# Performance work log

Hardware: AMD Instinct MI355X
Metric: run time of the kernel (lower is better)

Reference implementation:

```python
import jax, jax.numpy as jnp
import numpy as np

B = 1024       # batch of graphs
NUM = 512      # predicates / nodes per graph
D = 64         # embedding_dim
H = 64         # hidden_dim
E = 4096       # edges per graph (shared structure across batch)
MAIN_NUM = 10  # softmax segment [0, MAIN_NUM); sigmoid on the rest


def setup_inputs() -> dict:
    key = jax.random.key(0)
    ks = jax.random.split(key, 8)
    x = jax.random.uniform(ks[0], (B, NUM), dtype=jnp.float32)
    embedding = jax.random.normal(ks[1], (NUM, D), dtype=jnp.float32) * 0.1
    W1 = jax.random.normal(ks[2], (D, H), dtype=jnp.float32) * (1.0 / np.sqrt(D))
    b1 = jnp.zeros((H,), jnp.float32)
    W2 = jax.random.normal(ks[3], (H, H), dtype=jnp.float32) * (1.0 / np.sqrt(H))
    b2 = jnp.zeros((H,), jnp.float32)
    W3 = jax.random.normal(ks[4], (H, 1), dtype=jnp.float32) * (1.0 / np.sqrt(H))
    b3 = jnp.zeros((1,), jnp.float32)
    edge_row = jax.random.randint(ks[5], (E,), 0, NUM, dtype=jnp.int32)
    edge_col = jax.random.randint(ks[6], (E,), 0, NUM, dtype=jnp.int32)
    return {"x": x, "embedding": embedding, "W1": W1, "b1": b1,
            "W2": W2, "b2": b2, "W3": W3, "b3": b3,
            "edge_row": edge_row, "edge_col": edge_col}


def _gcn_layer(h, W, b, row, col, norm):
    # h: [B, NUM, in]; GCNConv = linear -> D^{-1/2} A D^{-1/2} aggregate -> +bias
    hW = jnp.einsum('bni,io->bno', h, W)                 # [B, NUM, out]
    msg = hW[:, row, :] * norm[None, :, None]            # [B, E, out]
    agg = jnp.zeros_like(hW).at[:, col, :].add(msg)      # scatter to targets
    return agg + b


def reference(x, embedding, W1, b1, W2, b2, W3, b3, edge_row, edge_col):
    num = x.shape[1]
    # symmetric GCN normalization (add_self_loops=False, unit edge weights)
    deg = jnp.zeros((num,), x.dtype).at[edge_col].add(1.0)
    dinv = jnp.where(deg > 0, jax.lax.rsqrt(jnp.maximum(deg, 1.0)), 0.0)
    norm = dinv[edge_row] * dinv[edge_col]               # [E]

    h = x[..., None] * embedding                         # [B, NUM, D]
    h = jax.nn.relu(_gcn_layer(h, W1, b1, edge_row, edge_col, norm))
    h = jax.nn.relu(_gcn_layer(h, W2, b2, edge_row, edge_col, norm))
    logits = _gcn_layer(h, W3, b3, edge_row, edge_col, norm)[..., 0]  # [B, NUM]

    # convert_to_confidence: softmax over multiclass segment, sigmoid elsewhere
    phi_sm = jax.nn.softmax(logits[:, :MAIN_NUM], axis=1)
    phi_sg = jax.nn.sigmoid(logits[:, MAIN_NUM:])
    return jnp.concatenate([phi_sm, phi_sg], axis=1)
```

## Files before the change

### kernel.cpp

```cpp
#include <hip/hip_runtime.h>
#include <stdint.h>

#define NB    1024
#define NUM   512
#define HD    64
#define NE    4096
#define NEP   4608
#define MAIN  10
#define HBS   72

typedef _Float16 hlf;
typedef __attribute__((ext_vector_type(2))) _Float16 hlf2;
typedef __attribute__((ext_vector_type(8))) _Float16 hlf8;
typedef __attribute__((ext_vector_type(4))) float f32x4;

__device__ __forceinline__ unsigned short f2h(float f) {
    hlf v = (hlf)f;
    return __builtin_bit_cast(unsigned short, v);
}

__global__ __launch_bounds__(512) void prep_all(
    const int* __restrict__ erow, const int* __restrict__ ecol,
    const float* __restrict__ emb, const float* __restrict__ W1,
    const float* __restrict__ W2,
    int* __restrict__ rsptr, int* __restrict__ colmap, int* __restrict__ epk,
    short* __restrict__ E1, short* __restrict__ W2T)
{
    const int t = threadIdx.x;
    if (blockIdx.x != 0) {
        int g = (blockIdx.x - 1) * 512 + t;
        if (g < NUM * HD) {
            int node = g >> 6, dim = g & 63;
            float acc = 0.0f;
            #pragma unroll
            for (int k = 0; k < HD; ++k) acc += emb[node * HD + k] * W1[k * HD + dim];
            E1[g] = (short)f2h(acc);
        } else if (g < NUM * HD + HD * HD) {
            int j = g - NUM * HD;
            int dout = j >> 6, din = j & 63;
            W2T[j] = (short)f2h(W2[din * HD + dout]);
        }
        return;
    }

    __shared__ int   sdeg[NUM];
    __shared__ int   aux[NUM];
    __shared__ float sdv[NUM];
    __shared__ int   rnk[NUM];
    __shared__ int   rdg[NUM];
    __shared__ int   wsum[8];

    const int lane = t & 63, wv = t >> 6;

    sdeg[t] = 0; aux[t] = 0;
    __syncthreads();
    for (int e = t; e < NE; e += 512) atomicAdd(&sdeg[ecol[e]], 1);
    __syncthreads();
    const int deg  = sdeg[t];
    const int pdeg = (deg + 1) & ~1;
    const int dbin = deg < NUM ? deg : NUM - 1;
    sdv[t] = deg > 0 ? rsqrtf((float)deg) : 0.0f;
    atomicAdd(&aux[dbin], 1);
    __syncthreads();
    {
        int v = aux[t];
        #pragma unroll
        for (int ofs = 1; ofs < 64; ofs <<= 1) {
            int sh = __shfl_up(v, ofs, 64);
            if (lane >= ofs) v += sh;
        }
        if (lane == 63) wsum[wv] = v;
        __syncthreads();
        if (t == 0) {
            int s = 0;
            #pragma unroll
            for (int w = 0; w < 8; ++w) { int tmp = wsum[w]; wsum[w] = s; s += tmp; }
        }
        __syncthreads();
        int inc = v + wsum[wv];
        aux[t]  = inc;
        __syncthreads();
        sdeg[t] = (t == 0) ? 0 : aux[t - 1];
        __syncthreads();
    }
    {
        int r = atomicAdd(&sdeg[dbin], 1);
        rnk[t] = r;
        rdg[r] = pdeg;
        colmap[r] = t;
    }
    __syncthreads();
    {
        int dv = rdg[t], v = dv;
        #pragma unroll
        for (int ofs = 1; ofs < 64; ofs <<= 1) {
            int sh = __shfl_up(v, ofs, 64);
            if (lane >= ofs) v += sh;
        }
        if (lane == 63) wsum[wv] = v;
        __syncthreads();
        if (t == 0) {
            int s = 0;
            #pragma unroll
            for (int w = 0; w < 8; ++w) { int tmp = wsum[w]; wsum[w] = s; s += tmp; }
        }
        __syncthreads();
        int inc  = v + wsum[wv];
        int excl = inc - dv;
        rsptr[t] = excl;
        if (t == NUM - 1) rsptr[NUM] = inc;
        aux[t] = excl;
        __syncthreads();
    }
    sdeg[t] = aux[rnk[t]];
    __syncthreads();
    for (int i = t; i < NEP; i += 512) epk[i] = 0;
    __syncthreads();
    for (int e = t; e < NE; e += 512) {
        int c = ecol[e], rr = erow[e];
        int p = atomicAdd(&sdeg[c], 1);
        unsigned ns = (unsigned)f2h(sdv[rr] * sdv[c]);
        epk[p] = (rr << 23) | (int)ns;
    }
}

__global__ __launch_bounds__(1024, 4) void gcn_body(
    const float* __restrict__ x, const hlf* __restrict__ E1,
    const hlf* __restrict__ W2T,
    const float* __restrict__ b1, const float* __restrict__ b2,
    const float* __restrict__ W3, const float* __restrict__ b3,
    const int* __restrict__ rsptrg, const int* __restrict__ colmap,
    const int* __restrict__ epkg,
    float* __restrict__ out)
{
    __shared__ hlf HA[NUM * HD];
    __shared__ hlf HB[NUM * HBS];
    __shared__ int eps[NEP + 8];
    __shared__ int sptr[513];
    __shared__ float sred[2];

    float* tv   = (float*)HB;
    float* slog = ((float*)HB) + NUM;

    const int t     = threadIdx.x;
    const int b     = blockIdx.x;
    const int lane  = t & 63;
    const int wave  = t >> 6;
    const int q     = lane >> 4;
    const int l15   = lane & 15;
    const int grp   = lane >> 3;
    const int dbase = (lane & 7) * 8;

    {
        const int4* g4 = (const int4*)epkg;
        *(int4*)&eps[t * 4] = g4[t];
        if (t < 128) *(int4*)&eps[4096 + t * 4] = g4[1024 + t];
        if (t < 8)   eps[NEP + t] = 0;
    }
    if (t < 513) sptr[t] = rsptrg[t];

    #pragma unroll
    for (int p = 0; p < 4; ++p) {
        int i = t + p * 1024;
        int r = i >> 3, d8 = (i & 7) * 8;
        float xr = x[b * NUM + r];
        hlf  xh = (hlf)xr;
        hlf8 e  = *(const hlf8*)&E1[r * HD + d8];
        hlf8 o;
        #pragma unroll
        for (int j = 0; j < 8; ++j) o[j] = e[j] * xh;
        *(hlf8*)&HA[r * HD + d8] = o;
    }

    float b1v[8], b2v[8], w3v[8];
    {
        f32x4 u0 = *(const f32x4*)&b1[dbase], u1 = *(const f32x4*)&b1[dbase + 4];
        f32x4 v0 = *(const f32x4*)&b2[dbase], v1 = *(const f32x4*)&b2[dbase + 4];
        f32x4 w0 = *(const f32x4*)&W3[dbase], w1 = *(const f32x4*)&W3[dbase + 4];
        #pragma unroll
        for (int j = 0; j < 4; ++j) {
            b1v[j] = u0[j]; b1v[j + 4] = u1[j];
            b2v[j] = v0[j]; b2v[j + 4] = v1[j];
            w3v[j] = w0[j]; w3v[j + 4] = w1[j];
        }
    }
    const char* HAb = (const char*)HA + dbase * 2;
    __syncthreads();

#define LDROW(d, pe) d = *(const uint4*)(HAb + ((unsigned)(pe) >> 16));
#define MACROW(hv, pe) {                                                      \
        const hlf nh = __builtin_bit_cast(hlf2, (unsigned)(pe))[0];           \
        const hlf2 p0 = __builtin_bit_cast(hlf2, (hv).x);                     \
        const hlf2 p1 = __builtin_bit_cast(hlf2, (hv).y);                     \
        const hlf2 p2 = __builtin_bit_cast(hlf2, (hv).z);                     \
        const hlf2 p3 = __builtin_bit_cast(hlf2, (hv).w);                     \
        a[0] = fmaf((float)p0[0], (float)nh, a[0]);                           \
        a[1] = fmaf((float)p0[1], (float)nh, a[1]);                           \
        a[2] = fmaf((float)p1[0], (float)nh, a[2]);                           \
        a[3] = fmaf((float)p1[1], (float)nh, a[3]);                           \
        a[4] = fmaf((float)p2[0], (float)nh, a[4]);                           \
        a[5] = fmaf((float)p2[1], (float)nh, a[5]);                           \
        a[6] = fmaf((float)p3[0], (float)nh, a[6]);                           \
        a[7] = fmaf((float)p3[1], (float)nh, a[7]); }

#define SPMM_PIPE(E0, E1v)                                                    \
    int e = E0;                                                               \
    int2 qa0 = *(const int2*)&eps[e], qb0 = *(const int2*)&eps[e + 2];        \
    uint4 u0, u1, u2, u3;                                                     \
    LDROW(u0, qa0.x) LDROW(u1, qa0.y) LDROW(u2, qb0.x) LDROW(u3, qb0.y)       \
    for (; e + 4 < E1v; e += 4) {                                             \
        int2 qa1 = *(const int2*)&eps[e + 4];                                 \
        int2 qb1 = *(const int2*)&eps[e + 6];                                 \
        uint4 w0, w1, w2, w3;                                                 \
        LDROW(w0, qa1.x) LDROW(w1, qa1.y) LDROW(w2, qb1.x) LDROW(w3, qb1.y)   \
        MACROW(u0, qa0.x) MACROW(u1, qa0.y)                                   \
        MACROW(u2, qb0.x) MACROW(u3, qb0.y)                                   \
        qa0 = qa1; qb0 = qb1; u0 = w0; u1 = w1; u2 = w2; u3 = w3;             \
    }                                                                         \
    if (e < E1v)     { MACROW(u0, qa0.x) MACROW(u1, qa0.y) }                  \
    if (e + 2 < E1v) { MACROW(u2, qb0.x) MACROW(u3, qb0.y) }

    #pragma unroll 1
    for (int set = 0; set < 4; ++set) {
        int wv8 = ((set & 1) ? (15 - wave) : wave) * 8;
        int r  = set * 128 + wv8 + grp;
        int e0 = sptr[r], e1 = sptr[r + 1];
        int c  = colmap[r];
        float a[8];
        #pragma unroll
        for (int j = 0; j < 8; ++j) a[j] = 0.0f;
        { SPMM_PIPE(e0, e1) }
        uint4 ov;
        ov.x = __builtin_bit_cast(unsigned, __builtin_amdgcn_cvt_pkrtz(
                   fmaxf(a[0] + b1v[0], 0.0f), fmaxf(a[1] + b1v[1], 0.0f)));
        ov.y = __builtin_bit_cast(unsigned, __builtin_amdgcn_cvt_pkrtz(
                   fmaxf(a[2] + b1v[2], 0.0f), fmaxf(a[3] + b1v[3], 0.0f)));
        ov.z = __builtin_bit_cast(unsigned, __builtin_amdgcn_cvt_pkrtz(
                   fmaxf(a[4] + b1v[4], 0.0f), fmaxf(a[5] + b1v[5], 0.0f)));
        ov.w = __builtin_bit_cast(unsigned, __builtin_amdgcn_cvt_pkrtz(
                   fmaxf(a[6] + b1v[6], 0.0f), fmaxf(a[7] + b1v[7], 0.0f)));
        *(uint4*)&HB[c * HBS + dbase] = ov;
    }
    __syncthreads();

    {
        hlf8 bfr[2][4];
        #pragma unroll
        for (int ks = 0; ks < 2; ++ks)
            #pragma unroll
            for (int nt = 0; nt < 4; ++nt)
                bfr[ks][nt] = *(const hlf8*)&W2T[(nt * 16 + l15) * HD + ks * 32 + q * 8];
        f32x4 acc[2][4];
        #pragma unroll
        for (int mt = 0; mt < 2; ++mt)
            #pragma unroll
            for (int nt = 0; nt < 4; ++nt) acc[mt][nt] = (f32x4){0.f, 0.f, 0.f, 0.f};
        const int mbase = wave * 32;
        #pragma unroll
        for (int mt = 0; mt < 2; ++mt)
            #pragma unroll
            for (int ks = 0; ks < 2; ++ks) {
                hlf8 af = *(const hlf8*)&HB[(mbase + mt * 16 + l15) * HBS
                                            + ks * 32 + q * 8];
                #pragma unroll
                for (int nt = 0; nt < 4; ++nt)
                    acc[mt][nt] = __builtin_amdgcn_mfma_f32_16x16x32_f16(
                        af, bfr[ks][nt], acc[mt][nt], 0, 0, 0);
            }
        #pragma unroll
        for (int mt = 0; mt < 2; ++mt)
            #pragma unroll
            for (int nt = 0; nt < 4; ++nt)
                #pragma unroll
                for (int i = 0; i < 4; ++i)
                    HA[(mbase + mt * 16 + q * 4 + i) * HD + nt * 16 + l15] =
                        (hlf)acc[mt][nt][i];
    }
    __syncthreads();

    #pragma unroll 1
    for (int set = 0; set < 4; ++set) {
        int wv8 = ((set & 1) ? (15 - wave) : wave) * 8;
        int r  = set * 128 + wv8 + grp;
        int e0 = sptr[r], e1 = sptr[r + 1];
        int c  = colmap[r];
        float a[8];
        #pragma unroll
        for (int j = 0; j < 8; ++j) a[j] = 0.0f;
        { SPMM_PIPE(e0, e1) }
        float v = 0.0f;
        #pragma unroll
        for (int j = 0; j < 8; ++j)
            v += fmaxf(a[j] + b2v[j], 0.0f) * w3v[j];
        v += __shfl_xor(v, 1, 64);
        v += __shfl_xor(v, 2, 64);
        v += __shfl_xor(v, 4, 64);
        if ((lane & 7) == 0) tv[c] = v;
    }
    __syncthreads();

    {
        int rk = t >> 1, hh = t & 1;
        int e0 = sptr[rk], e1 = sptr[rk + 1];
        int mid = (e0 + e1) >> 1;
        int ea = hh ? mid : e0;
        int eb = hh ? e1 : mid;
        float acc = 0.0f;
        for (int e = ea; e < eb; ++e) {
            unsigned pe = (unsigned)eps[e];
            float nf = (float)__builtin_bit_cast(hlf2, pe)[0];
            acc = fmaf(nf, *(const float*)((const char*)tv + (pe >> 21)), acc);
        }
        acc += __shfl_xor(acc, 1, 64);
        if (!hh) slog[colmap[rk]] = acc + b3[0];
    }
    __syncthreads();

    if (t < 64) {
        float v = (t < MAIN) ? slog[t] : -1e30f;
        float m = v;
        m = fmaxf(m, __shfl_xor(m, 1, 64));
        m = fmaxf(m, __shfl_xor(m, 2, 64));
        m = fmaxf(m, __shfl_xor(m, 4, 64));
        m = fmaxf(m, __shfl_xor(m, 8, 64));
        float ev = (t < MAIN) ? __expf(v - m) : 0.0f;
        ev += __shfl_xor(ev, 1, 64);
        ev += __shfl_xor(ev, 2, 64);
        ev += __shfl_xor(ev, 4, 64);
        ev += __shfl_xor(ev, 8, 64);
        if (t == 0) { sred[0] = m; sred[1] = ev; }
    }
    __syncthreads();

    if (t < NUM) {
        float l = slog[t];
        float o = (t < MAIN) ? __expf(l - sred[0]) / sred[1]
                             : 1.0f / (1.0f + __expf(-l));
        out[b * NUM + t] = o;
    }
#undef LDROW
#undef MACROW
#undef SPMM_PIPE
}

extern "C" void kernel_launch(void* const* d_in, const int* in_sizes, int n_in,
                              void* d_out, int out_size, void* d_ws, size_t ws_size,
                              hipStream_t stream) {
    const float* x    = (const float*)d_in[0];
    const float* emb  = (const float*)d_in[1];
    const float* W1   = (const float*)d_in[2];
    const float* b1   = (const float*)d_in[3];
    const float* W2   = (const float*)d_in[4];
    const float* b2   = (const float*)d_in[5];
    const float* W3   = (const float*)d_in[6];
    const float* b3   = (const float*)d_in[7];
    const int*   erow = (const int*)d_in[8];
    const int*   ecol = (const int*)d_in[9];

    char* ws = (char*)d_ws;
    int*   rsptr  = (int*)ws;
    int*   colmap = (int*)(ws + 2176);
    int*   epk    = (int*)(ws + 4224);
    short* E1     = (short*)(ws + 22656);
    short* W2T    = (short*)(ws + 88192);

    prep_all<<<73, 512, 0, stream>>>(erow, ecol, emb, W1, W2,
                                     rsptr, colmap, epk, E1, W2T);
    gcn_body<<<NB, 1024, 0, stream>>>(x, (const hlf*)E1, (const hlf*)W2T,
                                      b1, b2, W3, b3,
                                      rsptr, colmap, epk, (float*)d_out);
}
```

Baseline: 158.5 us.

## Reorder GCN stages to aggregate before transform and shrink shared memory

Layer 1 now gathers rows of the precomputed embedding·W1 table straight from global memory, scaling each edge by x times the edge norm, so the per-graph scaled embedding copy in LDS is no longer built. Layer 2 aggregates first and then runs the MFMA transform, fusing bias, ReLU and the W3 dot product into the MFMA epilogue, which removes the third SpMM over 64 features. Edge pointers, column map and degree are packed into one descriptor word, edges are read from global memory instead of being staged in LDS, and the row buffer uses an XOR swizzle instead of padding. Together these cut LDS use enough to raise the launch bound to 8 waves per SIMD, at the cost of more global and L2 gather traffic and the loss of the software-pipelined gather loop.

```diff
diff --git a/kernel.cpp b/kernel.cpp
--- a/kernel.cpp
+++ b/kernel.cpp
@@ -7,7 +7,6 @@
 #define NE    4096
 #define NEP   4608
 #define MAIN  10
-#define HBS   72
 
 typedef _Float16 hlf;
 typedef __attribute__((ext_vector_type(2))) _Float16 hlf2;
@@ -23,7 +22,7 @@
     const int* __restrict__ erow, const int* __restrict__ ecol,
     const float* __restrict__ emb, const float* __restrict__ W1,
     const float* __restrict__ W2,
-    int* __restrict__ rsptr, int* __restrict__ colmap, int* __restrict__ epk,
+    unsigned* __restrict__ desc, int* __restrict__ epk,
     short* __restrict__ E1, short* __restrict__ W2T)
 {
     const int t = threadIdx.x;
@@ -48,6 +47,7 @@
     __shared__ float sdv[NUM];
     __shared__ int   rnk[NUM];
     __shared__ int   rdg[NUM];
+    __shared__ int   scol[NUM];
     __shared__ int   wsum[8];
 
     const int lane = t & 63, wv = t >> 6;
@@ -87,7 +87,7 @@
         int r = atomicAdd(&sdeg[dbin], 1);
         rnk[t] = r;
         rdg[r] = pdeg;
-        colmap[r] = t;
+        scol[r] = t;
     }
     __syncthreads();
     {
@@ -107,8 +107,7 @@
         __syncthreads();
         int inc  = v + wsum[wv];
         int excl = inc - dv;
-        rsptr[t] = excl;
-        if (t == NUM - 1) rsptr[NUM] = inc;
+        desc[t] = (unsigned)excl | ((unsigned)scol[t] << 13) | ((unsigned)dv << 22);
         aux[t] = excl;
         __syncthreads();
     }
@@ -124,23 +123,20 @@
     }
 }
 
-__global__ __launch_bounds__(1024, 4) void gcn_body(
+__global__ __launch_bounds__(1024, 8) void gcn_body(
     const float* __restrict__ x, const hlf* __restrict__ E1,
     const hlf* __restrict__ W2T,
     const float* __restrict__ b1, const float* __restrict__ b2,
     const float* __restrict__ W3, const float* __restrict__ b3,
-    const int* __restrict__ rsptrg, const int* __restrict__ colmap,
-    const int* __restrict__ epkg,
+    const unsigned* __restrict__ descg, const int* __restrict__ epkg,
     float* __restrict__ out)
 {
-    __shared__ hlf HA[NUM * HD];
-    __shared__ hlf HB[NUM * HBS];
-    __shared__ int eps[NEP + 8];
-    __shared__ int sptr[513];
-    __shared__ float sred[2];
-
-    float* tv   = (float*)HB;
-    float* slog = ((float*)HB) + NUM;
+    __shared__ hlf   H[NUM * HD];
+    __shared__ float aux[NUM];
+    __shared__ hlf   xe[NEP];
+
+    float* slog = (float*)H;
+    float* sred = ((float*)H) + NUM;
 
     const int t     = threadIdx.x;
     const int b     = blockIdx.x;
@@ -149,170 +145,162 @@
     const int q     = lane >> 4;
     const int l15   = lane & 15;
     const int grp   = lane >> 3;
-    const int dbase = (lane & 7) * 8;
-
-    {
-        const int4* g4 = (const int4*)epkg;
-        *(int4*)&eps[t * 4] = g4[t];
-        if (t < 128) *(int4*)&eps[4096 + t * 4] = g4[1024 + t];
-        if (t < 8)   eps[NEP + t] = 0;
-    }
-    if (t < 513) sptr[t] = rsptrg[t];
-
-    #pragma unroll
-    for (int p = 0; p < 4; ++p) {
-        int i = t + p * 1024;
-        int r = i >> 3, d8 = (i & 7) * 8;
-        float xr = x[b * NUM + r];
-        hlf  xh = (hlf)xr;
-        hlf8 e  = *(const hlf8*)&E1[r * HD + d8];
-        hlf8 o;
-        #pragma unroll
-        for (int j = 0; j < 8; ++j) o[j] = e[j] * xh;
-        *(hlf8*)&HA[r * HD + d8] = o;
-    }
-
-    float b1v[8], b2v[8], w3v[8];
+    const int l7    = lane & 7;
+    const int dbase = l7 * 8;
+
+    if (t < NUM) aux[t] = x[b * NUM + t];
+    __syncthreads();
+    for (int i = t; i < NEP; i += 1024) {
+        unsigned pe = (unsigned)epkg[i];
+        float nf = (float)__builtin_bit_cast(hlf2, pe)[0];
+        xe[i] = (hlf)(nf * aux[pe >> 23]);
+    }
+
+    float b1v[8];
     {
         f32x4 u0 = *(const f32x4*)&b1[dbase], u1 = *(const f32x4*)&b1[dbase + 4];
-        f32x4 v0 = *(const f32x4*)&b2[dbase], v1 = *(const f32x4*)&b2[dbase + 4];
-        f32x4 w0 = *(const f32x4*)&W3[dbase], w1 = *(const f32x4*)&W3[dbase + 4];
-        #pragma unroll
-        for (int j = 0; j < 4; ++j) {
-            b1v[j] = u0[j]; b1v[j + 4] = u1[j];
-            b2v[j] = v0[j]; b2v[j + 4] = v1[j];
-            w3v[j] = w0[j]; w3v[j + 4] = w1[j];
-        }
-    }
-    const char* HAb = (const char*)HA + dbase * 2;
-    __syncthreads();
-
-#define LDROW(d, pe) d = *(const uint4*)(HAb + ((unsigned)(pe) >> 16));
-#define MACROW(hv, pe) {                                                      \
-        const hlf nh = __builtin_bit_cast(hlf2, (unsigned)(pe))[0];           \
+        #pragma unroll
+        for (int j = 0; j < 4; ++j) { b1v[j] = u0[j]; b1v[j + 4] = u1[j]; }
+    }
+    __syncthreads();
+
+#define MAC8(hv, sc) {                                                        \
         const hlf2 p0 = __builtin_bit_cast(hlf2, (hv).x);                     \
         const hlf2 p1 = __builtin_bit_cast(hlf2, (hv).y);                     \
         const hlf2 p2 = __builtin_bit_cast(hlf2, (hv).z);                     \
         const hlf2 p3 = __builtin_bit_cast(hlf2, (hv).w);                     \
-        a[0] = fmaf((float)p0[0], (float)nh, a[0]);                           \
-        a[1] = fmaf((float)p0[1], (float)nh, a[1]);                           \
-        a[2] = fmaf((float)p1[0], (float)nh, a[2]);                           \
-        a[3] = fmaf((float)p1[1], (float)nh, a[3]);                           \
-        a[4] = fmaf((float)p2[0], (float)nh, a[4]);                           \
-        a[5] = fmaf((float)p2[1], (float)nh, a[5]);                           \
-        a[6] = fmaf((float)p3[0], (float)nh, a[6]);                           \
-        a[7] = fmaf((float)p3[1], (float)nh, a[7]); }
-
-#define SPMM_PIPE(E0, E1v)                                                    \
-    int e = E0;                                                               \
-    int2 qa0 = *(const int2*)&eps[e], qb0 = *(const int2*)&eps[e + 2];        \
-    uint4 u0, u1, u2, u3;                                                     \
-    LDROW(u0, qa0.x) LDROW(u1, qa0.y) LDROW(u2, qb0.x) LDROW(u3, qb0.y)       \
-    for (; e + 4 < E1v; e += 4) {                                             \
-        int2 qa1 = *(const int2*)&eps[e + 4];                                 \
-        int2 qb1 = *(const int2*)&eps[e + 6];                                 \
-        uint4 w0, w1, w2, w3;                                                 \
-        LDROW(w0, qa1.x) LDROW(w1, qa1.y) LDROW(w2, qb1.x) LDROW(w3, qb1.y)   \
-        MACROW(u0, qa0.x) MACROW(u1, qa0.y)                                   \
-        MACROW(u2, qb0.x) MACROW(u3, qb0.y)                                   \
-        qa0 = qa1; qb0 = qb1; u0 = w0; u1 = w1; u2 = w2; u3 = w3;             \
-    }                                                                         \
-    if (e < E1v)     { MACROW(u0, qa0.x) MACROW(u1, qa0.y) }                  \
-    if (e + 2 < E1v) { MACROW(u2, qb0.x) MACROW(u3, qb0.y) }
-
-    #pragma unroll 1
-    for (int set = 0; set < 4; ++set) {
-        int wv8 = ((set & 1) ? (15 - wave) : wave) * 8;
-        int r  = set * 128 + wv8 + grp;
-        int e0 = sptr[r], e1 = sptr[r + 1];
-        int c  = colmap[r];
-        float a[8];
-        #pragma unroll
-        for (int j = 0; j < 8; ++j) a[j] = 0.0f;
-        { SPMM_PIPE(e0, e1) }
-        uint4 ov;
-        ov.x = __builtin_bit_cast(unsigned, __builtin_amdgcn_cvt_pkrtz(
-                   fmaxf(a[0] + b1v[0], 0.0f), fmaxf(a[1] + b1v[1], 0.0f)));
-        ov.y = __builtin_bit_cast(unsigned, __builtin_amdgcn_cvt_pkrtz(
-                   fmaxf(a[2] + b1v[2], 0.0f), fmaxf(a[3] + b1v[3], 0.0f)));
-        ov.z = __builtin_bit_cast(unsigned, __builtin_amdgcn_cvt_pkrtz(
-                   fmaxf(a[4] + b1v[4], 0.0f), fmaxf(a[5] + b1v[5], 0.0f)));
-        ov.w = __builtin_bit_cast(unsigned, __builtin_amdgcn_cvt_pkrtz(
-                   fmaxf(a[6] + b1v[6], 0.0f), fmaxf(a[7] + b1v[7], 0.0f)));
-        *(uint4*)&HB[c * HBS + dbase] = ov;
-    }
-    __syncthreads();
-
-    {
-        hlf8 bfr[2][4];
-        #pragma unroll
-        for (int ks = 0; ks < 2; ++ks)
-            #pragma unroll
-            for (int nt = 0; nt < 4; ++nt)
-                bfr[ks][nt] = *(const hlf8*)&W2T[(nt * 16 + l15) * HD + ks * 32 + q * 8];
-        f32x4 acc[2][4];
+        a[0] = fmaf((float)p0[0], (float)(sc), a[0]);                         \
+        a[1] = fmaf((float)p0[1], (float)(sc), a[1]);                         \
+        a[2] = fmaf((float)p1[0], (float)(sc), a[2]);                         \
+        a[3] = fmaf((float)p1[1], (float)(sc), a[3]);                         \
+        a[4] = fmaf((float)p2[0], (float)(sc), a[4]);                         \
+        a[5] = fmaf((float)p2[1], (float)(sc), a[5]);                         \
+        a[6] = fmaf((float)p3[0], (float)(sc), a[6]);                         \
+        a[7] = fmaf((float)p3[1], (float)(sc), a[7]); }
+
+    {
+        const char* E1b = (const char*)E1 + dbase * 2;
+        #pragma unroll 1
+        for (int set = 0; set < 4; ++set) {
+            int r = set * 128 + wave * 8 + grp;
+            unsigned d = descg[r];
+            int e0 = d & 8191, c = (d >> 13) & 511, e1 = e0 + (d >> 22);
+            float a[8];
+            #pragma unroll
+            for (int j = 0; j < 8; ++j) a[j] = 0.0f;
+            for (int e = e0; e < e1; e += 2) {
+                int2 qp = *(const int2*)&epkg[e];
+                hlf2 xs = *(const hlf2*)&xe[e];
+                uint4 g0 = *(const uint4*)(E1b + ((unsigned)qp.x >> 16));
+                uint4 g1 = *(const uint4*)(E1b + ((unsigned)qp.y >> 16));
+                MAC8(g0, xs[0]); MAC8(g1, xs[1]);
+            }
+            uint4 ov;
+            ov.x = __builtin_bit_cast(unsigned, __builtin_amdgcn_cvt_pkrtz(
+                       fmaxf(a[0] + b1v[0], 0.0f), fmaxf(a[1] + b1v[1], 0.0f)));
+            ov.y = __builtin_bit_cast(unsigned, __builtin_amdgcn_cvt_pkrtz(
+                       fmaxf(a[2] + b1v[2], 0.0f), fmaxf(a[3] + b1v[3], 0.0f)));
+            ov.z = __builtin_bit_cast(unsigned, __builtin_amdgcn_cvt_pkrtz(
+                       fmaxf(a[4] + b1v[4], 0.0f), fmaxf(a[5] + b1v[5], 0.0f)));
+            ov.w = __builtin_bit_cast(unsigned, __builtin_amdgcn_cvt_pkrtz(
+                       fmaxf(a[6] + b1v[6], 0.0f), fmaxf(a[7] + b1v[7], 0.0f)));
+            *(uint4*)&H[c * HD + dbase] = ov;
+        }
+    }
+    __syncthreads();
+
+    {
+        const char* Hb = (const char*)H + dbase * 2;
+        uint4 agg[4]; int cset[4];
+        #pragma unroll 1
+        for (int set = 0; set < 4; ++set) {
+            int r = set * 128 + wave * 8 + grp;
+            unsigned d = descg[r];
+            int e0 = d & 8191, c = (d >> 13) & 511, e1 = e0 + (d >> 22);
+            float a[8];
+            #pragma unroll
+            for (int j = 0; j < 8; ++j) a[j] = 0.0f;
+            for (int e = e0; e < e1; e += 2) {
+                int2 qp = *(const int2*)&epkg[e];
+                uint4 g0 = *(const uint4*)(Hb + ((unsigned)qp.x >> 16));
+                uint4 g1 = *(const uint4*)(Hb + ((unsigned)qp.y >> 16));
+                MAC8(g0, __builtin_bit_cast(hlf2, (unsigned)qp.x)[0]);
+                MAC8(g1, __builtin_bit_cast(hlf2, (unsigned)qp.y)[0]);
+            }
+            uint4 ov;
+            ov.x = __builtin_bit_cast(unsigned, __builtin_amdgcn_cvt_pkrtz(a[0], a[1]));
+            ov.y = __builtin_bit_cast(unsigned, __builtin_amdgcn_cvt_pkrtz(a[2], a[3]));
+            ov.z = __builtin_bit_cast(unsigned, __builtin_amdgcn_cvt_pkrtz(a[4], a[5]));
+            ov.w = __builtin_bit_cast(unsigned, __builtin_amdgcn_cvt_pkrtz(a[6], a[7]));
+            agg[set] = ov; cset[set] = c;
+        }
+        __syncthreads();
+        #pragma unroll
+        for (int set = 0; set < 4; ++set) {
+            int c = cset[set];
+            *(uint4*)((char*)H + c * 128 + ((dbase * 2) ^ ((c & 7) << 4))) = agg[set];
+        }
+    }
+    __syncthreads();
+
+    {
+        const int mbase = wave * 32;
+        const int sw0 = (q * 16) ^ ((l15 & 7) << 4);
+        const int sw1 = (64 + q * 16) ^ ((l15 & 7) << 4);
+        const char* rb0 = (const char*)H + (mbase + l15) * 128;
+        const char* rb1 = rb0 + 16 * 128;
+        hlf8 a00 = *(const hlf8*)(rb0 + sw0), a01 = *(const hlf8*)(rb0 + sw1);
+        hlf8 a10 = *(const hlf8*)(rb1 + sw0), a11 = *(const hlf8*)(rb1 + sw1);
+        float tp[2][4];
+        #pragma unroll
+        for (int i = 0; i < 4; ++i) { tp[0][i] = 0.0f; tp[1][i] = 0.0f; }
+        #pragma unroll
+        for (int nt = 0; nt < 4; ++nt) {
+            int col = nt * 16 + l15;
+            hlf8 bf0 = *(const hlf8*)&W2T[col * HD + q * 8];
+            hlf8 bf1 = *(const hlf8*)&W2T[col * HD + 32 + q * 8];
+            f32x4 acc0 = (f32x4){0.f, 0.f, 0.f, 0.f};
+            f32x4 acc1 = (f32x4){0.f, 0.f, 0.f, 0.f};
+            acc0 = __builtin_amdgcn_mfma_f32_16x16x32_f16(a00, bf0, acc0, 0, 0, 0);
+            acc0 = __builtin_amdgcn_mfma_f32_16x16x32_f16(a01, bf1, acc0, 0, 0, 0);
+            acc1 = __builtin_amdgcn_mfma_f32_16x16x32_f16(a10, bf0, acc1, 0, 0, 0);
+            acc1 = __builtin_amdgcn_mfma_f32_16x16x32_f16(a11, bf1, acc1, 0, 0, 0);
+            float bc = b2[col], wc = W3[col];
+            #pragma unroll
+            for (int i = 0; i < 4; ++i) {
+                tp[0][i] += fmaxf(acc0[i] + bc, 0.0f) * wc;
+                tp[1][i] += fmaxf(acc1[i] + bc, 0.0f) * wc;
+            }
+        }
         #pragma unroll
         for (int mt = 0; mt < 2; ++mt)
             #pragma unroll
-            for (int nt = 0; nt < 4; ++nt) acc[mt][nt] = (f32x4){0.f, 0.f, 0.f, 0.f};
-        const int mbase = wave * 32;
-        #pragma unroll
-        for (int mt = 0; mt < 2; ++mt)
-            #pragma unroll
-            for (int ks = 0; ks < 2; ++ks) {
-                hlf8 af = *(const hlf8*)&HB[(mbase + mt * 16 + l15) * HBS
-                                            + ks * 32 + q * 8];
-                #pragma unroll
-                for (int nt = 0; nt < 4; ++nt)
-                    acc[mt][nt] = __builtin_amdgcn_mfma_f32_16x16x32_f16(
-                        af, bfr[ks][nt], acc[mt][nt], 0, 0, 0);
+            for (int i = 0; i < 4; ++i) {
+                float v = tp[mt][i];
+                v += __shfl_xor(v, 1, 64);
+                v += __shfl_xor(v, 2, 64);
+                v += __shfl_xor(v, 4, 64);
+                v += __shfl_xor(v, 8, 64);
+                if (l15 == 0) aux[mbase + mt * 16 + q * 4 + i] = v;
             }
-        #pragma unroll
-        for (int mt = 0; mt < 2; ++mt)
-            #pragma unroll
-            for (int nt = 0; nt < 4; ++nt)
-                #pragma unroll
-                for (int i = 0; i < 4; ++i)
-                    HA[(mbase + mt * 16 + q * 4 + i) * HD + nt * 16 + l15] =
-                        (hlf)acc[mt][nt][i];
-    }
-    __syncthreads();
-
-    #pragma unroll 1
-    for (int set = 0; set < 4; ++set) {
-        int wv8 = ((set & 1) ? (15 - wave) : wave) * 8;
-        int r  = set * 128 + wv8 + grp;
-        int e0 = sptr[r], e1 = sptr[r + 1];
-        int c  = colmap[r];
-        float a[8];
-        #pragma unroll
-        for (int j = 0; j < 8; ++j) a[j] = 0.0f;
-        { SPMM_PIPE(e0, e1) }
-        float v = 0.0f;
-        #pragma unroll
-        for (int j = 0; j < 8; ++j)
-            v += fmaxf(a[j] + b2v[j], 0.0f) * w3v[j];
-        v += __shfl_xor(v, 1, 64);
-        v += __shfl_xor(v, 2, 64);
-        v += __shfl_xor(v, 4, 64);
-        if ((lane & 7) == 0) tv[c] = v;
     }
     __syncthreads();
 
     {
         int rk = t >> 1, hh = t & 1;
-        int e0 = sptr[rk], e1 = sptr[rk + 1];
-        int mid = (e0 + e1) >> 1;
+        unsigned d = descg[rk];
+        int e0 = d & 8191, c = (d >> 13) & 511, deg = d >> 22;
+        int mid = e0 + (deg >> 1);
         int ea = hh ? mid : e0;
-        int eb = hh ? e1 : mid;
+        int eb = hh ? e0 + deg : mid;
         float acc = 0.0f;
         for (int e = ea; e < eb; ++e) {
-            unsigned pe = (unsigned)eps[e];
+            unsigned pe = (unsigned)epkg[e];
             float nf = (float)__builtin_bit_cast(hlf2, pe)[0];
-            acc = fmaf(nf, *(const float*)((const char*)tv + (pe >> 21)), acc);
+            acc = fmaf(nf, aux[pe >> 23], acc);
         }
         acc += __shfl_xor(acc, 1, 64);
-        if (!hh) slog[colmap[rk]] = acc + b3[0];
+        if (!hh) slog[c] = acc + b3[0];
     }
     __syncthreads();
 
@@ -338,9 +326,7 @@
                              : 1.0f / (1.0f + __expf(-l));
         out[b * NUM + t] = o;
     }
-#undef LDROW
-#undef MACROW
-#undef SPMM_PIPE
+#undef MAC8
 }
 
 extern "C" void kernel_launch(void* const* d_in, const int* in_sizes, int n_in,
@@ -358,15 +344,14 @@
     const int*   ecol = (const int*)d_in[9];
 
     char* ws = (char*)d_ws;
-    int*   rsptr  = (int*)ws;
-    int*   colmap = (int*)(ws + 2176);
+    unsigned* desc = (unsigned*)ws;
     int*   epk    = (int*)(ws + 4224);
     short* E1     = (short*)(ws + 22656);
     short* W2T    = (short*)(ws + 88192);
 
     prep_all<<<73, 512, 0, stream>>>(erow, ecol, emb, W1, W2,
-                                     rsptr, colmap, epk, E1, W2T);
+                                     desc, epk, E1, W2T);
     gcn_body<<<NB, 1024, 0, stream>>>(x, (const hlf*)E1, (const hlf*)W2T,
                                       b1, b2, W3, b3,
-                                      rsptr, colmap, epk, (float*)d_out);
+                                      desc, epk, (float*)d_out);
 }
```

Result: slower. 170.5 us (+7.5%).

## Replace sparse gather aggregation with dense MFMA adjacency matmul

Applied to the files above, without the earlier changes.

Builds a dense normalized adjacency matrix (512x512) in the prep kernel via atomics, converts it to fp16 in an MFMA fragment layout, and computes the first two GCN aggregations as dense matrix multiplies on the matrix cores instead of per-edge LDS gathers. Node features are now stored transposed with XOR swizzling in LDS, and the layer-2 linear plus W3 projection are fused into one MFMA pass. This trades the irregular sparse gathers for about 64x more arithmetic (dense 512x512 versus 4096 edges). It also adds a memset and an extra cast kernel, and the dense fragments of S are streamed from global memory by every block.

```diff
diff --git a/kernel.cpp b/kernel.cpp
--- a/kernel.cpp
+++ b/kernel.cpp
@@ -7,7 +7,6 @@
 #define NE    4096
 #define NEP   4608
 #define MAIN  10
-#define HBS   72
 
 typedef _Float16 hlf;
 typedef __attribute__((ext_vector_type(2))) _Float16 hlf2;
@@ -24,17 +23,18 @@
     const float* __restrict__ emb, const float* __restrict__ W1,
     const float* __restrict__ W2,
     int* __restrict__ rsptr, int* __restrict__ colmap, int* __restrict__ epk,
-    short* __restrict__ E1, short* __restrict__ W2T)
+    short* __restrict__ E1T, short* __restrict__ W2T,
+    float* __restrict__ S32)
 {
     const int t = threadIdx.x;
     if (blockIdx.x != 0) {
         int g = (blockIdx.x - 1) * 512 + t;
         if (g < NUM * HD) {
-            int node = g >> 6, dim = g & 63;
+            int dim = g >> 9, node = g & 511;
             float acc = 0.0f;
             #pragma unroll
             for (int k = 0; k < HD; ++k) acc += emb[node * HD + k] * W1[k * HD + dim];
-            E1[g] = (short)f2h(acc);
+            E1T[g] = (short)f2h(acc);
         } else if (g < NUM * HD + HD * HD) {
             int j = g - NUM * HD;
             int dout = j >> 6, din = j & 63;
@@ -119,200 +119,217 @@
     for (int e = t; e < NE; e += 512) {
         int c = ecol[e], rr = erow[e];
         int p = atomicAdd(&sdeg[c], 1);
-        unsigned ns = (unsigned)f2h(sdv[rr] * sdv[c]);
-        epk[p] = (rr << 23) | (int)ns;
-    }
+        float nf = sdv[rr] * sdv[c];
+        unsigned ns = (unsigned)f2h(nf);
+        epk[p] = (rr << 16) | (int)ns;
+        atomicAdd(&S32[c * NUM + rr], nf);
+    }
+}
+
+__global__ __launch_bounds__(1024) void cast_S(
+    const float* __restrict__ S32, hlf* __restrict__ Sfr)
+{
+    int idx = blockIdx.x * 1024 + threadIdx.x;
+    int f = idx >> 6, l = idx & 63;
+    int mt = f >> 4, kt = f & 15;
+    int c  = mt * 16 + (l & 15);
+    int r0 = kt * 32 + (l >> 4) * 8;
+    const float* src = S32 + c * NUM + r0;
+    hlf8 o;
+    #pragma unroll
+    for (int j = 0; j < 8; ++j) o[j] = (hlf)src[j];
+    *(hlf8*)(Sfr + idx * 8) = o;
 }
 
 __global__ __launch_bounds__(1024, 4) void gcn_body(
-    const float* __restrict__ x, const hlf* __restrict__ E1,
-    const hlf* __restrict__ W2T,
+    const float* __restrict__ x, const hlf* __restrict__ E1T,
+    const hlf* __restrict__ W2T, const hlf* __restrict__ Sfr,
     const float* __restrict__ b1, const float* __restrict__ b2,
     const float* __restrict__ W3, const float* __restrict__ b3,
-    const int* __restrict__ rsptrg, const int* __restrict__ colmap,
+    const int* __restrict__ rsptrg, const int* __restrict__ cmapg,
     const int* __restrict__ epkg,
     float* __restrict__ out)
 {
-    __shared__ hlf HA[NUM * HD];
-    __shared__ hlf HB[NUM * HBS];
-    __shared__ int eps[NEP + 8];
-    __shared__ int sptr[513];
+    __shared__ hlf   HT[HD * NUM];
+    __shared__ hlf   AG[HD * NUM];
+    __shared__ float xs[NUM];
+    __shared__ float tv[NUM];
+    __shared__ float slog[NUM];
     __shared__ float sred[2];
 
-    float* tv   = (float*)HB;
-    float* slog = ((float*)HB) + NUM;
-
-    const int t     = threadIdx.x;
-    const int b     = blockIdx.x;
-    const int lane  = t & 63;
-    const int wave  = t >> 6;
-    const int q     = lane >> 4;
-    const int l15   = lane & 15;
-    const int grp   = lane >> 3;
-    const int dbase = (lane & 7) * 8;
-
-    {
-        const int4* g4 = (const int4*)epkg;
-        *(int4*)&eps[t * 4] = g4[t];
-        if (t < 128) *(int4*)&eps[4096 + t * 4] = g4[1024 + t];
-        if (t < 8)   eps[NEP + t] = 0;
-    }
-    if (t < 513) sptr[t] = rsptrg[t];
+    const int t    = threadIdx.x;
+    const int b    = blockIdx.x;
+    const int lane = t & 63;
+    const int wave = t >> 6;
+    const int q    = lane >> 4;
+    const int l15  = lane & 15;
+
+    if (t < NUM) xs[t] = x[b * NUM + t];
+    __syncthreads();
 
     #pragma unroll
     for (int p = 0; p < 4; ++p) {
         int i = t + p * 1024;
-        int r = i >> 3, d8 = (i & 7) * 8;
-        float xr = x[b * NUM + r];
-        hlf  xh = (hlf)xr;
-        hlf8 e  = *(const hlf8*)&E1[r * HD + d8];
+        int d = i >> 6, r0 = (i & 63) * 8;
+        hlf8 ev = *(const hlf8*)&E1T[d * NUM + r0];
         hlf8 o;
         #pragma unroll
-        for (int j = 0; j < 8; ++j) o[j] = e[j] * xh;
-        *(hlf8*)&HA[r * HD + d8] = o;
-    }
-
-    float b1v[8], b2v[8], w3v[8];
-    {
-        f32x4 u0 = *(const f32x4*)&b1[dbase], u1 = *(const f32x4*)&b1[dbase + 4];
-        f32x4 v0 = *(const f32x4*)&b2[dbase], v1 = *(const f32x4*)&b2[dbase + 4];
-        f32x4 w0 = *(const f32x4*)&W3[dbase], w1 = *(const f32x4*)&W3[dbase + 4];
-        #pragma unroll
-        for (int j = 0; j < 4; ++j) {
-            b1v[j] = u0[j]; b1v[j + 4] = u1[j];
-            b2v[j] = v0[j]; b2v[j + 4] = v1[j];
-            w3v[j] = w0[j]; w3v[j + 4] = w1[j];
-        }
-    }
-    const char* HAb = (const char*)HA + dbase * 2;
-    __syncthreads();
-
-#define LDROW(d, pe) d = *(const uint4*)(HAb + ((unsigned)(pe) >> 16));
-#define MACROW(hv, pe) {                                                      \
-        const hlf nh = __builtin_bit_cast(hlf2, (unsigned)(pe))[0];           \
-        const hlf2 p0 = __builtin_bit_cast(hlf2, (hv).x);                     \
-        const hlf2 p1 = __builtin_bit_cast(hlf2, (hv).y);                     \
-        const hlf2 p2 = __builtin_bit_cast(hlf2, (hv).z);                     \
-        const hlf2 p3 = __builtin_bit_cast(hlf2, (hv).w);                     \
-        a[0] = fmaf((float)p0[0], (float)nh, a[0]);                           \
-        a[1] = fmaf((float)p0[1], (float)nh, a[1]);                           \
-        a[2] = fmaf((float)p1[0], (float)nh, a[2]);                           \
-        a[3] = fmaf((float)p1[1], (float)nh, a[3]);                           \
-        a[4] = fmaf((float)p2[0], (float)nh, a[4]);                           \
-        a[5] = fmaf((float)p2[1], (float)nh, a[5]);                           \
-        a[6] = fmaf((float)p3[0], (float)nh, a[6]);                           \
-        a[7] = fmaf((float)p3[1], (float)nh, a[7]); }
-
-#define SPMM_PIPE(E0, E1v)                                                    \
-    int e = E0;                                                               \
-    int2 qa0 = *(const int2*)&eps[e], qb0 = *(const int2*)&eps[e + 2];        \
-    uint4 u0, u1, u2, u3;                                                     \
-    LDROW(u0, qa0.x) LDROW(u1, qa0.y) LDROW(u2, qb0.x) LDROW(u3, qb0.y)       \
-    for (; e + 4 < E1v; e += 4) {                                             \
-        int2 qa1 = *(const int2*)&eps[e + 4];                                 \
-        int2 qb1 = *(const int2*)&eps[e + 6];                                 \
-        uint4 w0, w1, w2, w3;                                                 \
-        LDROW(w0, qa1.x) LDROW(w1, qa1.y) LDROW(w2, qb1.x) LDROW(w3, qb1.y)   \
-        MACROW(u0, qa0.x) MACROW(u1, qa0.y)                                   \
-        MACROW(u2, qb0.x) MACROW(u3, qb0.y)                                   \
-        qa0 = qa1; qb0 = qb1; u0 = w0; u1 = w1; u2 = w2; u3 = w3;             \
-    }                                                                         \
-    if (e < E1v)     { MACROW(u0, qa0.x) MACROW(u1, qa0.y) }                  \
-    if (e + 2 < E1v) { MACROW(u2, qb0.x) MACROW(u3, qb0.y) }
-
-    #pragma unroll 1
-    for (int set = 0; set < 4; ++set) {
-        int wv8 = ((set & 1) ? (15 - wave) : wave) * 8;
-        int r  = set * 128 + wv8 + grp;
-        int e0 = sptr[r], e1 = sptr[r + 1];
-        int c  = colmap[r];
-        float a[8];
-        #pragma unroll
-        for (int j = 0; j < 8; ++j) a[j] = 0.0f;
-        { SPMM_PIPE(e0, e1) }
-        uint4 ov;
-        ov.x = __builtin_bit_cast(unsigned, __builtin_amdgcn_cvt_pkrtz(
-                   fmaxf(a[0] + b1v[0], 0.0f), fmaxf(a[1] + b1v[1], 0.0f)));
-        ov.y = __builtin_bit_cast(unsigned, __builtin_amdgcn_cvt_pkrtz(
-                   fmaxf(a[2] + b1v[2], 0.0f), fmaxf(a[3] + b1v[3], 0.0f)));
-        ov.z = __builtin_bit_cast(unsigned, __builtin_amdgcn_cvt_pkrtz(
-                   fmaxf(a[4] + b1v[4], 0.0f), fmaxf(a[5] + b1v[5], 0.0f)));
-        ov.w = __builtin_bit_cast(unsigned, __builtin_amdgcn_cvt_pkrtz(
-                   fmaxf(a[6] + b1v[6], 0.0f), fmaxf(a[7] + b1v[7], 0.0f)));
-        *(uint4*)&HB[c * HBS + dbase] = ov;
-    }
-    __syncthreads();
-
-    {
-        hlf8 bfr[2][4];
-        #pragma unroll
-        for (int ks = 0; ks < 2; ++ks)
+        for (int j = 0; j < 8; ++j) o[j] = ev[j] * (hlf)xs[r0 + j];
+        *(hlf8*)((char*)HT + d * 1024 + ((r0 * 2) ^ ((d & 7) << 4))) = o;
+    }
+
+    float b1l[4], b2l[4], w3l[4];
+    #pragma unroll
+    for (int nt = 0; nt < 4; ++nt) {
+        b1l[nt] = b1[nt * 16 + l15];
+        b2l[nt] = b2[nt * 16 + l15];
+        w3l[nt] = W3[nt * 16 + l15];
+    }
+    __syncthreads();
+
+    {
+        f32x4 acc[2][4];
+        #pragma unroll
+        for (int mm = 0; mm < 2; ++mm)
+            #pragma unroll
+            for (int nt = 0; nt < 4; ++nt) acc[mm][nt] = (f32x4){0.f, 0.f, 0.f, 0.f};
+        #pragma unroll
+        for (int kt = 0; kt < 16; ++kt) {
+            hlf8 bf[4];
+            #pragma unroll
+            for (int nt = 0; nt < 4; ++nt) {
+                int row = nt * 16 + l15;
+                bf[nt] = *(const hlf8*)((const char*)HT + row * 1024 +
+                             ((kt * 64 + q * 16) ^ ((row & 7) << 4)));
+            }
+            #pragma unroll
+            for (int mm = 0; mm < 2; ++mm) {
+                hlf8 af = *(const hlf8*)((const char*)Sfr +
+                              (((wave * 2 + mm) * 16 + kt) << 10) + lane * 16);
+                #pragma unroll
+                for (int nt = 0; nt < 4; ++nt)
+                    acc[mm][nt] = __builtin_amdgcn_mfma_f32_16x16x32_f16(
+                        af, bf[nt], acc[mm][nt], 0, 0, 0);
+            }
+        }
+        #pragma unroll
+        for (int mm = 0; mm < 2; ++mm) {
+            int mt = wave * 2 + mm;
+            #pragma unroll
+            for (int nt = 0; nt < 4; ++nt) {
+                int n = nt * 16 + l15;
+                uint2 pk;
+                pk.x = __builtin_bit_cast(unsigned, __builtin_amdgcn_cvt_pkrtz(
+                           fmaxf(acc[mm][nt][0] + b1l[nt], 0.0f),
+                           fmaxf(acc[mm][nt][1] + b1l[nt], 0.0f)));
+                pk.y = __builtin_bit_cast(unsigned, __builtin_amdgcn_cvt_pkrtz(
+                           fmaxf(acc[mm][nt][2] + b1l[nt], 0.0f),
+                           fmaxf(acc[mm][nt][3] + b1l[nt], 0.0f)));
+                *(uint2*)((char*)AG + n * 1024 +
+                          ((mt * 32 + q * 8) ^ ((n & 7) << 4))) = pk;
+            }
+        }
+    }
+    __syncthreads();
+
+    {
+        f32x4 acc[2][4];
+        #pragma unroll
+        for (int mm = 0; mm < 2; ++mm)
+            #pragma unroll
+            for (int nt = 0; nt < 4; ++nt) acc[mm][nt] = (f32x4){0.f, 0.f, 0.f, 0.f};
+        #pragma unroll
+        for (int kt = 0; kt < 16; ++kt) {
+            hlf8 bf[4];
+            #pragma unroll
+            for (int nt = 0; nt < 4; ++nt) {
+                int row = nt * 16 + l15;
+                bf[nt] = *(const hlf8*)((const char*)AG + row * 1024 +
+                             ((kt * 64 + q * 16) ^ ((row & 7) << 4)));
+            }
+            #pragma unroll
+            for (int mm = 0; mm < 2; ++mm) {
+                hlf8 af = *(const hlf8*)((const char*)Sfr +
+                              (((wave * 2 + mm) * 16 + kt) << 10) + lane * 16);
+                #pragma unroll
+                for (int nt = 0; nt < 4; ++nt)
+                    acc[mm][nt] = __builtin_amdgcn_mfma_f32_16x16x32_f16(
+                        af, bf[nt], acc[mm][nt], 0, 0, 0);
+            }
+        }
+        __syncthreads();
+        #pragma unroll
+        for (int mm = 0; mm < 2; ++mm) {
+            #pragma unroll
+            for (int nt = 0; nt < 4; ++nt) {
+                int n = nt * 16 + l15;
+                #pragma unroll
+                for (int i = 0; i < 4; ++i) {
+                    int m = (wave * 2 + mm) * 16 + q * 4 + i;
+                    *(hlf*)((char*)HT + m * 128 + ((n * 2) ^ ((m & 7) << 4))) =
+                        (hlf)acc[mm][nt][i];
+                }
+            }
+        }
+    }
+    __syncthreads();
+
+    {
+        hlf8 wb[2][4];
+        #pragma unroll
+        for (int kt = 0; kt < 2; ++kt)
             #pragma unroll
             for (int nt = 0; nt < 4; ++nt)
-                bfr[ks][nt] = *(const hlf8*)&W2T[(nt * 16 + l15) * HD + ks * 32 + q * 8];
-        f32x4 acc[2][4];
-        #pragma unroll
-        for (int mt = 0; mt < 2; ++mt)
-            #pragma unroll
-            for (int nt = 0; nt < 4; ++nt) acc[mt][nt] = (f32x4){0.f, 0.f, 0.f, 0.f};
-        const int mbase = wave * 32;
-        #pragma unroll
-        for (int mt = 0; mt < 2; ++mt)
-            #pragma unroll
-            for (int ks = 0; ks < 2; ++ks) {
-                hlf8 af = *(const hlf8*)&HB[(mbase + mt * 16 + l15) * HBS
-                                            + ks * 32 + q * 8];
+                wb[kt][nt] = *(const hlf8*)&W2T[(nt * 16 + l15) * HD + kt * 32 + q * 8];
+        #pragma unroll
+        for (int mm = 0; mm < 2; ++mm) {
+            int mt = wave * 2 + mm;
+            f32x4 z[4];
+            #pragma unroll
+            for (int nt = 0; nt < 4; ++nt) z[nt] = (f32x4){0.f, 0.f, 0.f, 0.f};
+            #pragma unroll
+            for (int kt = 0; kt < 2; ++kt) {
+                int m = mt * 16 + l15;
+                hlf8 af = *(const hlf8*)((const char*)HT + m * 128 +
+                              ((kt * 64 + q * 16) ^ ((m & 7) << 4)));
                 #pragma unroll
                 for (int nt = 0; nt < 4; ++nt)
-                    acc[mt][nt] = __builtin_amdgcn_mfma_f32_16x16x32_f16(
-                        af, bfr[ks][nt], acc[mt][nt], 0, 0, 0);
-            }
-        #pragma unroll
-        for (int mt = 0; mt < 2; ++mt)
+                    z[nt] = __builtin_amdgcn_mfma_f32_16x16x32_f16(
+                        af, wb[kt][nt], z[nt], 0, 0, 0);
+            }
+            float vs[4] = {0.f, 0.f, 0.f, 0.f};
             #pragma unroll
             for (int nt = 0; nt < 4; ++nt)
                 #pragma unroll
                 for (int i = 0; i < 4; ++i)
-                    HA[(mbase + mt * 16 + q * 4 + i) * HD + nt * 16 + l15] =
-                        (hlf)acc[mt][nt][i];
-    }
-    __syncthreads();
-
-    #pragma unroll 1
-    for (int set = 0; set < 4; ++set) {
-        int wv8 = ((set & 1) ? (15 - wave) : wave) * 8;
-        int r  = set * 128 + wv8 + grp;
-        int e0 = sptr[r], e1 = sptr[r + 1];
-        int c  = colmap[r];
-        float a[8];
-        #pragma unroll
-        for (int j = 0; j < 8; ++j) a[j] = 0.0f;
-        { SPMM_PIPE(e0, e1) }
-        float v = 0.0f;
-        #pragma unroll
-        for (int j = 0; j < 8; ++j)
-            v += fmaxf(a[j] + b2v[j], 0.0f) * w3v[j];
-        v += __shfl_xor(v, 1, 64);
-        v += __shfl_xor(v, 2, 64);
-        v += __shfl_xor(v, 4, 64);
-        if ((lane & 7) == 0) tv[c] = v;
+                    vs[i] += fmaxf(z[nt][i] + b2l[nt], 0.0f) * w3l[nt];
+            #pragma unroll
+            for (int i = 0; i < 4; ++i) {
+                float v = vs[i];
+                v += __shfl_xor(v, 1, 64);
+                v += __shfl_xor(v, 2, 64);
+                v += __shfl_xor(v, 4, 64);
+                v += __shfl_xor(v, 8, 64);
+                if (l15 == 0) tv[mt * 16 + q * 4 + i] = v;
+            }
+        }
     }
     __syncthreads();
 
     {
         int rk = t >> 1, hh = t & 1;
-        int e0 = sptr[rk], e1 = sptr[rk + 1];
+        int e0 = rsptrg[rk], e1 = rsptrg[rk + 1];
         int mid = (e0 + e1) >> 1;
         int ea = hh ? mid : e0;
         int eb = hh ? e1 : mid;
         float acc = 0.0f;
         for (int e = ea; e < eb; ++e) {
-            unsigned pe = (unsigned)eps[e];
+            unsigned pe = (unsigned)epkg[e];
             float nf = (float)__builtin_bit_cast(hlf2, pe)[0];
-            acc = fmaf(nf, *(const float*)((const char*)tv + (pe >> 21)), acc);
+            acc = fmaf(nf, tv[pe >> 16], acc);
         }
         acc += __shfl_xor(acc, 1, 64);
-        if (!hh) slog[colmap[rk]] = acc + b3[0];
+        if (!hh) slog[cmapg[rk]] = acc + b3[0];
     }
     __syncthreads();
 
@@ -338,9 +355,6 @@
                              : 1.0f / (1.0f + __expf(-l));
         out[b * NUM + t] = o;
     }
-#undef LDROW
-#undef MACROW
-#undef SPMM_PIPE
 }
 
 extern "C" void kernel_launch(void* const* d_in, const int* in_sizes, int n_in,
@@ -358,15 +372,19 @@
     const int*   ecol = (const int*)d_in[9];
 
     char* ws = (char*)d_ws;
-    int*   rsptr  = (int*)ws;
-    int*   colmap = (int*)(ws + 2176);
-    int*   epk    = (int*)(ws + 4224);
-    short* E1     = (short*)(ws + 22656);
-    short* W2T    = (short*)(ws + 88192);
-
+    float* S32   = (float*)ws;
+    short* Sfr   = (short*)(ws + 1048576);
+    short* E1T   = (short*)(ws + 1572864);
+    short* W2T   = (short*)(ws + 1638400);
+    int*   epk   = (int*)(ws + 1646592);
+    int*   rsptr = (int*)(ws + 1665024);
+    int*   colmap= (int*)(ws + 1667200);
+
+    hipMemsetAsync(S32, 0, NUM * NUM * sizeof(float), stream);
     prep_all<<<73, 512, 0, stream>>>(erow, ecol, emb, W1, W2,
-                                     rsptr, colmap, epk, E1, W2T);
-    gcn_body<<<NB, 1024, 0, stream>>>(x, (const hlf*)E1, (const hlf*)W2T,
-                                      b1, b2, W3, b3,
+                                     rsptr, colmap, epk, E1T, W2T, S32);
+    cast_S<<<32, 1024, 0, stream>>>(S32, (hlf*)Sfr);
+    gcn_body<<<NB, 1024, 0, stream>>>(x, (const hlf*)E1T, (const hlf*)W2T,
+                                      (const hlf*)Sfr, b1, b2, W3, b3,
                                       rsptr, colmap, epk, (float*)d_out);
 }
```

Measured after the change: 180.6 us. +13.9%, slower.
